# Kernel tuning notes

Hardware: AMD Instinct MI355X
Metric: run time of the kernel (lower is better)

Reference implementation:

```python
import jax, jax.numpy as jnp
import numpy as np

N, E = 50000, 800000          # nodes, edges
IN, H, C = 256, 4, 64          # in_channels, heads, per-head out channels
HID, OUT = 64, 40              # lin1 hidden, num classes
NEG_SLOPE = 0.2                # PyG GATConv default


def setup_inputs() -> dict:
    key = jax.random.key(0)
    ks = jax.random.split(key, 10)
    s = 0.05
    return {
        "x": jax.random.normal(ks[0], (N, IN), jnp.float32),
        "edge_index": jax.random.randint(ks[1], (2, E), 0, N, dtype=jnp.int64),
        "W": jax.random.normal(ks[2], (IN, H * C), jnp.float32) * s,     # GATConv lin (no bias)
        "att_src": jax.random.normal(ks[3], (H, C), jnp.float32) * s,
        "att_dst": jax.random.normal(ks[4], (H, C), jnp.float32) * s,
        "bias_conv": jnp.zeros((H * C,), jnp.float32),
        "W1": jax.random.normal(ks[5], (H * C, HID), jnp.float32) * s,
        "b1": jnp.zeros((HID,), jnp.float32),
        "W2": jax.random.normal(ks[6], (HID, OUT), jnp.float32) * s,
        "b2": jnp.zeros((OUT,), jnp.float32),
    }


def reference(x, edge_index, W, att_src, att_dst, bias_conv, W1, b1, W2, b2):
    n = x.shape[0]
    # PyG GATConv default: add self-loops (also guarantees no empty segments)
    loop = jnp.arange(n, dtype=edge_index.dtype)
    src = jnp.concatenate([edge_index[0], loop])  # [E+N]
    dst = jnp.concatenate([edge_index[1], loop])

    h = (x @ W).reshape(n, H, C)                         # [N,H,C]
    a_src = jnp.einsum('nhc,hc->nh', h, att_src)         # [N,H]
    a_dst = jnp.einsum('nhc,hc->nh', h, att_dst)

    # per-edge attention logits + segment softmax over incoming edges of dst
    e = jax.nn.leaky_relu(a_src[src] + a_dst[dst], NEG_SLOPE)   # [E+N,H]
    m = jax.ops.segment_max(e, dst, num_segments=n)             # [N,H]
    ex = jnp.exp(e - m[dst])
    denom = jax.ops.segment_sum(ex, dst, num_segments=n)
    alpha = ex / denom[dst]                                     # [E+N,H]

    # weighted scatter-aggregate of source features
    msg = alpha[:, :, None] * h[src]                            # [E+N,H,C]
    out = jax.ops.segment_sum(msg, dst, num_segments=n)         # [N,H,C]
    out = out.reshape(n, H * C) + bias_conv

    out = jax.nn.relu(out)              # .relu() after conv1 (dropout off in eval)
    out = jax.nn.relu(out @ W1 + b1)    # lin1 + relu
    return out @ W2 + b2                # lin2
```

## Files before the change

kernel.cpp:

```cpp
#include <hip/hip_runtime.h>
#include <math.h>

#define HEADS 4
#define CH 64
#define HC 256
#define SLOPE 0.2f

typedef __attribute__((ext_vector_type(8))) short bf16x8;
typedef __attribute__((ext_vector_type(4))) float f32x4;

__device__ __forceinline__ float4 ld4(const float* p){ return *(const float4*)p; }
__device__ __forceinline__ void st4(float* p, float4 v){ *(float4*)p = v; }
__device__ __forceinline__ float lrelu(float x){ return x > 0.f ? x : SLOPE * x; }
__device__ __forceinline__ unsigned short f2bf(float f){
  union { float f; unsigned int u; } v; v.f = f;
  unsigned int r = v.u + 0x7fffu + ((v.u >> 16) & 1u);
  return (unsigned short)(r >> 16);
}
__device__ __forceinline__ float bflo(unsigned int u){
  union { unsigned int u; float f; } v; v.u = u << 16; return v.f;
}
__device__ __forceinline__ float bfhi(unsigned int u){
  union { unsigned int u; float f; } v; v.u = u & 0xffff0000u; return v.f;
}
__device__ __forceinline__ void split2(float v, unsigned short& h, unsigned short& l){
  unsigned int u = __float_as_uint(v);
  h = (unsigned short)(u >> 16);
  float hf = __uint_as_float(u & 0xffff0000u);
  l = (unsigned short)(__float_as_uint(v - hf) >> 16);
}
__device__ __forceinline__ void dma16(const unsigned short* g, unsigned short* l){
  __builtin_amdgcn_global_load_lds(
      (const __attribute__((address_space(1))) unsigned int*)g,
      (__attribute__((address_space(3))) unsigned int*)l, 16, 0, 0);
}

__global__ __launch_bounds__(256) void k_pre(const float* __restrict__ x,
    const float* __restrict__ W, const float* __restrict__ W1, const float* __restrict__ W2,
    unsigned short* __restrict__ Ahi, unsigned short* __restrict__ Alo,
    unsigned short* __restrict__ Bhi, unsigned short* __restrict__ Blo,
    unsigned short* __restrict__ W1h, unsigned short* __restrict__ W1l,
    unsigned short* __restrict__ W2h, unsigned short* __restrict__ W2l,
    const int* __restrict__ ei, int* __restrict__ count,
    int nf4, int E, int nSplit) {
  int b = blockIdx.x, t = threadIdx.x;
  if (b < nSplit) {
    int idx = b*256 + t;
    if (idx < nf4) {
      float4 v = ld4(&x[(size_t)idx*4]);
      ushort4 h, l;
      split2(v.x, h.x, l.x); split2(v.y, h.y, l.y);
      split2(v.z, h.z, l.z); split2(v.w, h.w, l.w);
      *(ushort4*)&Ahi[(size_t)idx*4] = h;
      *(ushort4*)&Alo[(size_t)idx*4] = l;
    }
  } else if (b < nSplit + 256) {
    int nn = b - nSplit;
    unsigned short h, l;
    split2(W[(size_t)t*256 + nn], h, l);
    Bhi[(size_t)nn*256 + t] = h; Blo[(size_t)nn*256 + t] = l;
  } else if (b < nSplit + 320) {
    int nn = b - nSplit - 256;
    unsigned short h, l;
    split2(W1[(size_t)t*64 + nn], h, l);
    W1h[(size_t)nn*256 + t] = h; W1l[(size_t)nn*256 + t] = l;
  } else if (b < nSplit + 368) {
    if (t < 64) {
      int nn = b - nSplit - 320;
      float v = (nn < 40) ? W2[(size_t)t*40 + nn] : 0.f;
      unsigned short h, l;
      split2(v, h, l);
      W2h[(size_t)nn*64 + t] = h; W2l[(size_t)nn*64 + t] = l;
    }
  } else {
    int e = (b - nSplit - 368)*256 + t;
    if (e < E) atomicAdd(&count[ei[E+e]], 1);
  }
}

__global__ __launch_bounds__(256) void k_scan1(const int* __restrict__ count,
    int* __restrict__ excl, int* __restrict__ partial, int n) {
  __shared__ int sd[256];
  int blk = blockIdx.x, t = threadIdx.x;
  int i = blk*256 + t;
  int v = (i < n) ? count[i] + 1 : 0;
  sd[t] = v; __syncthreads();
  for (int off=1; off<256; off<<=1) {
    int xx = (t >= off) ? sd[t-off] : 0;
    __syncthreads();
    sd[t] += xx;
    __syncthreads();
  }
  if (i < n) excl[i] = sd[t] - v;
  if (t == 255) partial[blk] = sd[255];
}

__global__ __launch_bounds__(256) void k_scan23(int* __restrict__ row_start,
    int* __restrict__ cursor, const int* __restrict__ partial,
    const int* __restrict__ count, int n, int nb) {
  __shared__ int sd[256];
  int b = blockIdx.x, t = threadIdx.x;
  int v = (t < nb) ? partial[t] : 0;
  sd[t] = v; __syncthreads();
  for (int off=1; off<256; off<<=1) {
    int xx = (t >= off) ? sd[t-off] : 0;
    __syncthreads();
    sd[t] += xx;
    __syncthreads();
  }
  int pb = (b > 0) ? sd[b-1] : 0;
  int i = b*256 + t;
  if (i < n) {
    int vv = row_start[i] + pb;
    row_start[i] = vv;
    cursor[i] = vv;
    if (i == n-1) row_start[n] = vv + count[i] + 1;
  }
}

__global__ __launch_bounds__(256, 4) void k_gemmfill(const unsigned short* __restrict__ Ahi,
    const unsigned short* __restrict__ Alo,
    const unsigned short* __restrict__ Bhi_t, const unsigned short* __restrict__ Blo_t,
    unsigned short* __restrict__ hbf,
    const float* __restrict__ att_src, const float* __restrict__ att_dst,
    float* __restrict__ a_srcO, float* __restrict__ a_dstO, int M, int nGemm,
    const int* __restrict__ ei, int* __restrict__ cursor, int* __restrict__ csr,
    int E, int EN) {
  __shared__ __align__(16) unsigned short L[4*4096];
  int t = threadIdx.x;
  int b = blockIdx.x;
  if (b >= nGemm) {
    int base = (b - nGemm)*1024 + t;
    int e0 = base, e1 = base + 256, e2 = base + 512, e3 = base + 768;
    bool q0 = e0 < EN, q1 = e1 < EN, q2 = e2 < EN, q3 = e3 < EN;
    int s0=0,d0=0,s1=0,d1=0,s2=0,d2=0,s3=0,d3=0;
    if (q0) { if (e0 < E) { s0 = ei[e0]; d0 = ei[E+e0]; } else { s0 = e0-E; d0 = s0; } }
    if (q1) { if (e1 < E) { s1 = ei[e1]; d1 = ei[E+e1]; } else { s1 = e1-E; d1 = s1; } }
    if (q2) { if (e2 < E) { s2 = ei[e2]; d2 = ei[E+e2]; } else { s2 = e2-E; d2 = s2; } }
    if (q3) { if (e3 < E) { s3 = ei[e3]; d3 = ei[E+e3]; } else { s3 = e3-E; d3 = s3; } }
    if (q0) { int p = atomicAdd(&cursor[d0], 1); csr[p] = s0; }
    if (q1) { int p = atomicAdd(&cursor[d1], 1); csr[p] = s1; }
    if (q2) { int p = atomicAdd(&cursor[d2], 1); csr[p] = s2; }
    if (q3) { int p = atomicAdd(&cursor[d3], 1); csr[p] = s3; }
    return;
  }
  int lane = t & 63, w = t >> 6;
  int wr = w >> 1, wc = w & 1;
  int ln15 = lane & 15, lq = lane >> 4;
  int row0 = (b >> 1) * 128, col0 = (b & 1) * 128;

  f32x4 acc[4][4];
  #pragma unroll
  for (int i=0;i<4;i++)
    #pragma unroll
    for (int j=0;j<4;j++) acc[i][j] = (f32x4){0.f,0.f,0.f,0.f};

  int sA = w*128 + lane;
  int sB = sA + 64;
  int RA = sA>>3, uA = (sA&7)^(RA&7), idxA = (RA<<1)|(uA&1), segA = uA>>1;
  int RB = sB>>3, uB = (sB&7)^(RB&7), idxB = (RB<<1)|(uB&1), segB = uB>>1;
  size_t gA_a = (size_t)(row0+idxA)*256 + segA*8;
  size_t gA_b = (size_t)(row0+idxB)*256 + segB*8;
  size_t gB_a = (size_t)(col0+idxA)*256 + segA*8;
  size_t gB_b = (size_t)(col0+idxB)*256 + segB*8;
  int l0 = (w*128)*8, l1 = (w*128+64)*8;

  for (int c = 0; c < 8; c++) {
    int k0 = c*32;
    dma16(Ahi   + gA_a + k0, &L[0*4096 + l0]);
    dma16(Ahi   + gA_b + k0, &L[0*4096 + l1]);
    dma16(Alo   + gA_a + k0, &L[1*4096 + l0]);
    dma16(Alo   + gA_b + k0, &L[1*4096 + l1]);
    dma16(Bhi_t + gB_a + k0, &L[2*4096 + l0]);
    dma16(Bhi_t + gB_b + k0, &L[2*4096 + l1]);
    dma16(Blo_t + gB_a + k0, &L[3*4096 + l0]);
    dma16(Blo_t + gB_b + k0, &L[3*4096 + l1]);
    __syncthreads();

    bf16x8 bh[4], bl[4];
    #pragma unroll
    for (int j = 0; j < 4; j++) {
      int nn = wc*64 + j*16 + ln15;
      int R = nn >> 1, u = (lq << 1) | (nn & 1);
      int s = R*8 + (u ^ (R & 7));
      bh[j] = *(bf16x8*)&L[2*4096 + s*8];
      bl[j] = *(bf16x8*)&L[3*4096 + s*8];
    }
    #pragma unroll
    for (int i = 0; i < 4; i++) {
      int r = wr*64 + i*16 + ln15;
      int R = r >> 1, u = (lq << 1) | (r & 1);
      int s = R*8 + (u ^ (R & 7));
      bf16x8 ah = *(bf16x8*)&L[0*4096 + s*8];
      bf16x8 al = *(bf16x8*)&L[1*4096 + s*8];
      #pragma unroll
      for (int j = 0; j < 4; j++) {
        acc[i][j] = __builtin_amdgcn_mfma_f32_16x16x32_bf16(ah, bh[j], acc[i][j], 0,0,0);
        acc[i][j] = __builtin_amdgcn_mfma_f32_16x16x32_bf16(al, bh[j], acc[i][j], 0,0,0);
        acc[i][j] = __builtin_amdgcn_mfma_f32_16x16x32_bf16(ah, bl[j], acc[i][j], 0,0,0);
      }
    }
    __syncthreads();
  }
  unsigned short* hb2 = hbf + (size_t)(b & 1) * M * 128;
  #pragma unroll
  for (int i = 0; i < 4; i++) {
    #pragma unroll
    for (int r = 0; r < 4; r++) {
      int row = row0 + wr*64 + i*16 + lq*4 + r;
      if (row < M) {
        #pragma unroll
        for (int j = 0; j < 4; j++) {
          int col = wc*64 + j*16 + ln15;
          hb2[(size_t)row*128 + col] = f2bf(acc[i][j][r]);
        }
      }
    }
  }
  int head = (b & 1)*2 + wc;
  float asv[4], adv[4];
  #pragma unroll
  for (int j=0;j<4;j++){
    asv[j] = att_src[head*CH + j*16 + ln15];
    adv[j] = att_dst[head*CH + j*16 + ln15];
  }
  #pragma unroll
  for (int i = 0; i < 4; i++) {
    #pragma unroll
    for (int r = 0; r < 4; r++) {
      float ps = acc[i][0][r]*asv[0] + acc[i][1][r]*asv[1]
               + acc[i][2][r]*asv[2] + acc[i][3][r]*asv[3];
      float pd = acc[i][0][r]*adv[0] + acc[i][1][r]*adv[1]
               + acc[i][2][r]*adv[2] + acc[i][3][r]*adv[3];
      #pragma unroll
      for (int m=8; m>=1; m>>=1) { ps += __shfl_xor(ps, m); pd += __shfl_xor(pd, m); }
      if (ln15 == 0) {
        int row = row0 + wr*64 + i*16 + lq*4 + r;
        if (row < M) { a_srcO[row*4+head] = ps; a_dstO[row*4+head] = pd; }
      }
    }
  }
}

__global__ __launch_bounds__(256) void k_gat(const unsigned short* __restrict__ hbf,
    const float* __restrict__ a_src, const float* __restrict__ a_dst,
    const int* __restrict__ row_start, const int* __restrict__ csr,
    const float* __restrict__ bias, unsigned short* __restrict__ outbf,
    int N, int nBlk) {
  int w = threadIdx.x >> 6, lane = threadIdx.x & 63;
  int q = lane >> 4, cl = lane & 15;
  int pass = (blockIdx.x >= nBlk) ? 1 : 0;
  int blk = blockIdx.x - pass*nBlk;
  int n = blk*16 + w*4 + q;
  int c0 = cl * 8;
  int hd = cl >> 3;
  int eb = q * 16;
  const unsigned short* hb = hbf + (size_t)pass * N * 128;

  __shared__ float s_p[4][64][2];

  float2 ad = *(const float2*)&a_dst[(size_t)n*4 + pass*2];
  float dsum = 0.f;
  float acc[8];
  #pragma unroll
  for (int k=0;k<8;k++) acc[k]=0.f;

  int beg = row_start[n];
  int deg = row_start[n+1] - beg;
  int dm = max(deg, __shfl_xor(deg, 16));
  dm = max(dm, __shfl_xor(dm, 32));

  for (int cb = 0; cb < dm; cb += 16) {
    int cnt = min(16, deg - cb);
    int cm  = min(16, dm - cb);
    int s = 0;
    float p0 = 0.f, p1 = 0.f;
    if (cl < cnt) {
      s = csr[beg + cb + cl];
      float2 as = *(const float2*)&a_src[(size_t)s*4 + pass*2];
      p0 = __expf(lrelu(as.x + ad.x));
      p1 = __expf(lrelu(as.y + ad.y));
    }
    *(float2*)&s_p[w][eb + cl][0] = make_float2(p0, p1);

    bool v0 = 0 < cnt, v1 = 1 < cnt, v2 = 2 < cnt, v3 = 3 < cnt;
    uint4 u0 = make_uint4(0,0,0,0), u1 = u0, u2 = u0, u3 = u0;
    int ss;
    ss = __shfl(s, eb + 0); if (v0) u0 = *(const uint4*)&hb[(size_t)ss*128 + c0];
    ss = __shfl(s, eb + 1); if (v1) u1 = *(const uint4*)&hb[(size_t)ss*128 + c0];
    ss = __shfl(s, eb + 2); if (v2) u2 = *(const uint4*)&hb[(size_t)ss*128 + c0];
    ss = __shfl(s, eb + 3); if (v3) u3 = *(const uint4*)&hb[(size_t)ss*128 + c0];
    for (int g = 0; g < cm; g += 4) {
      int f0 = g+4, f1 = g+5, f2 = g+6, f3 = g+7;
      bool w0 = f0 < cnt, w1 = f1 < cnt, w2 = f2 < cnt, w3 = f3 < cnt;
      uint4 t0 = make_uint4(0,0,0,0), t1 = t0, t2 = t0, t3 = t0;
      ss = __shfl(s, eb + (f0 & 15)); if (w0) t0 = *(const uint4*)&hb[(size_t)ss*128 + c0];
      ss = __shfl(s, eb + (f1 & 15)); if (w1) t1 = *(const uint4*)&hb[(size_t)ss*128 + c0];
      ss = __shfl(s, eb + (f2 & 15)); if (w2) t2 = *(const uint4*)&hb[(size_t)ss*128 + c0];
      ss = __shfl(s, eb + (f3 & 15)); if (w3) t3 = *(const uint4*)&hb[(size_t)ss*128 + c0];
      if (v0) {
        float pw = s_p[w][eb + g    ][hd]; dsum += pw;
        acc[0] += pw*bflo(u0.x); acc[1] += pw*bfhi(u0.x);
        acc[2] += pw*bflo(u0.y); acc[3] += pw*bfhi(u0.y);
        acc[4] += pw*bflo(u0.z); acc[5] += pw*bfhi(u0.z);
        acc[6] += pw*bflo(u0.w); acc[7] += pw*bfhi(u0.w);
      }
      if (v1) {
        float pw = s_p[w][eb + g + 1][hd]; dsum += pw;
        acc[0] += pw*bflo(u1.x); acc[1] += pw*bfhi(u1.x);
        acc[2] += pw*bflo(u1.y); acc[3] += pw*bfhi(u1.y);
        acc[4] += pw*bflo(u1.z); acc[5] += pw*bfhi(u1.z);
        acc[6] += pw*bflo(u1.w); acc[7] += pw*bfhi(u1.w);
      }
      if (v2) {
        float pw = s_p[w][eb + g + 2][hd]; dsum += pw;
        acc[0] += pw*bflo(u2.x); acc[1] += pw*bfhi(u2.x);
        acc[2] += pw*bflo(u2.y); acc[3] += pw*bfhi(u2.y);
        acc[4] += pw*bflo(u2.z); acc[5] += pw*bfhi(u2.z);
        acc[6] += pw*bflo(u2.w); acc[7] += pw*bfhi(u2.w);
      }
      if (v3) {
        float pw = s_p[w][eb + g + 3][hd]; dsum += pw;
        acc[0] += pw*bflo(u3.x); acc[1] += pw*bfhi(u3.x);
        acc[2] += pw*bflo(u3.y); acc[3] += pw*bfhi(u3.y);
        acc[4] += pw*bflo(u3.z); acc[5] += pw*bfhi(u3.z);
        acc[6] += pw*bflo(u3.w); acc[7] += pw*bfhi(u3.w);
      }
      u0 = t0; u1 = t1; u2 = t2; u3 = t3;
      v0 = w0; v1 = w1; v2 = w2; v3 = w3;
    }
  }
  float inv = 1.f / dsum;
  float4 b0 = ld4(&bias[pass*128 + c0]);
  float4 b1 = ld4(&bias[pass*128 + c0 + 4]);
  uint4 o;
  o.x = (unsigned)f2bf(fmaxf(acc[0]*inv + b0.x, 0.f))
      | ((unsigned)f2bf(fmaxf(acc[1]*inv + b0.y, 0.f)) << 16);
  o.y = (unsigned)f2bf(fmaxf(acc[2]*inv + b0.z, 0.f))
      | ((unsigned)f2bf(fmaxf(acc[3]*inv + b0.w, 0.f)) << 16);
  o.z = (unsigned)f2bf(fmaxf(acc[4]*inv + b1.x, 0.f))
      | ((unsigned)f2bf(fmaxf(acc[5]*inv + b1.y, 0.f)) << 16);
  o.w = (unsigned)f2bf(fmaxf(acc[6]*inv + b1.z, 0.f))
      | ((unsigned)f2bf(fmaxf(acc[7]*inv + b1.w, 0.f)) << 16);
  *(uint4*)&outbf[(size_t)n*HC + pass*128 + c0] = o;
}

__global__ __launch_bounds__(256) void k_mlp(const unsigned short* __restrict__ Cbf,
    const unsigned short* __restrict__ W1h, const unsigned short* __restrict__ W1l,
    const unsigned short* __restrict__ W2h, const unsigned short* __restrict__ W2l,
    const float* __restrict__ b1, const float* __restrict__ b2,
    float* __restrict__ out, int M) {
  __shared__ __align__(16) unsigned short Abuf[4096];
  __shared__ __align__(16) unsigned short Hs[128*72];
  int t = threadIdx.x, lane = t & 63, w = t >> 6;
  int ln15 = lane & 15, lq = lane >> 4;
  int row0 = blockIdx.x * 128;

  f32x4 acc1[2][4];
  #pragma unroll
  for (int i=0;i<2;i++)
    #pragma unroll
    for (int j=0;j<4;j++) acc1[i][j] = (f32x4){0.f,0.f,0.f,0.f};

  int sA = w*64 + lane;
  int sB = 256 + w*64 + lane;
  int rA = sA >> 2, segA = (sA & 3) ^ ((rA >> 1) & 3);
  int rB = sB >> 2, segB = (sB & 3) ^ ((rB >> 1) & 3);
  size_t gA = (size_t)(row0 + rA) * 256 + segA*8;
  size_t gB = (size_t)(row0 + rB) * 256 + segB*8;
  int lA = (w*64)*8, lB = (256 + w*64)*8;

  for (int c = 0; c < 8; c++) {
    int k0 = c*32;
    dma16(Cbf + gA + k0, &Abuf[lA]);
    dma16(Cbf + gB + k0, &Abuf[lB]);
    __syncthreads();
    bf16x8 a[2];
    #pragma unroll
    for (int i = 0; i < 2; i++) {
      int r = w*32 + i*16 + ln15;
      int s = r*4 + (lq ^ ((r >> 1) & 3));
      a[i] = *(bf16x8*)&Abuf[s*8];
    }
    #pragma unroll
    for (int j = 0; j < 4; j++) {
      int n = j*16 + ln15;
      int k = k0 + lq*8;
      bf16x8 bh = *(const bf16x8*)&W1h[(size_t)n*256 + k];
      bf16x8 bl = *(const bf16x8*)&W1l[(size_t)n*256 + k];
      #pragma unroll
      for (int i = 0; i < 2; i++) {
        acc1[i][j] = __builtin_amdgcn_mfma_f32_16x16x32_bf16(a[i], bh, acc1[i][j], 0,0,0);
        acc1[i][j] = __builtin_amdgcn_mfma_f32_16x16x32_bf16(a[i], bl, acc1[i][j], 0,0,0);
      }
    }
    __syncthreads();
  }
  #pragma unroll
  for (int j = 0; j < 4; j++) {
    int col = j*16 + ln15;
    float bv = b1[col];
    #pragma unroll
    for (int i = 0; i < 2; i++) {
      #pragma unroll
      for (int r = 0; r < 4; r++) {
        int row = w*32 + i*16 + lq*4 + r;
        Hs[row*72 + col] = f2bf(fmaxf(acc1[i][j][r] + bv, 0.f));
      }
    }
  }
  f32x4 acc2[2][3];
  #pragma unroll
  for (int i=0;i<2;i++)
    #pragma unroll
    for (int j=0;j<3;j++) acc2[i][j] = (f32x4){0.f,0.f,0.f,0.f};
  #pragma unroll
  for (int kf = 0; kf < 2; kf++) {
    bf16x8 a2[2];
    #pragma unroll
    for (int i = 0; i < 2; i++) {
      int m = w*32 + i*16 + ln15;
      a2[i] = *(bf16x8*)&Hs[m*72 + kf*32 + lq*8];
    }
    #pragma unroll
    for (int j = 0; j < 3; j++) {
      int n = j*16 + ln15;
      int k = kf*32 + lq*8;
      bf16x8 wh = *(const bf16x8*)&W2h[(size_t)n*64 + k];
      bf16x8 wl = *(const bf16x8*)&W2l[(size_t)n*64 + k];
      #pragma unroll
      for (int i = 0; i < 2; i++) {
        acc2[i][j] = __builtin_amdgcn_mfma_f32_16x16x32_bf16(a2[i], wh, acc2[i][j], 0,0,0);
        acc2[i][j] = __builtin_amdgcn_mfma_f32_16x16x32_bf16(a2[i], wl, acc2[i][j], 0,0,0);
      }
    }
  }
  #pragma unroll
  for (int j = 0; j < 3; j++) {
    int col = j*16 + ln15;
    if (col < 40) {
      float bv = b2[col];
      #pragma unroll
      for (int i = 0; i < 2; i++) {
        #pragma unroll
        for (int r = 0; r < 4; r++) {
          int row = row0 + w*32 + i*16 + lq*4 + r;
          if (row < M) out[(size_t)row*40 + col] = acc2[i][j][r] + bv;
        }
      }
    }
  }
}

extern "C" void kernel_launch(void* const* d_in, const int* in_sizes, int n_in,
                              void* d_out, int out_size, void* d_ws, size_t ws_size,
                              hipStream_t stream) {
  const int Nn = in_sizes[0] / HC;
  const int E  = in_sizes[1] / 2;
  const int Mpad = (Nn + 127) & ~127;
  const float* x        = (const float*)d_in[0];
  const int*   ei       = (const int*)d_in[1];
  const float* W        = (const float*)d_in[2];
  const float* att_src  = (const float*)d_in[3];
  const float* att_dst  = (const float*)d_in[4];
  const float* biasconv = (const float*)d_in[5];
  const float* W1       = (const float*)d_in[6];
  const float* b1       = (const float*)d_in[7];
  const float* W2       = (const float*)d_in[8];
  const float* b2       = (const float*)d_in[9];
  float* out = (float*)d_out;

  size_t off = 0;
  auto alloc = [&](size_t bytes)->void* {
    void* p = (void*)((char*)d_ws + off);
    off += (bytes + 255) & ~(size_t)255;
    return p;
  };
  unsigned short* hbf = (unsigned short*)alloc((size_t)Nn*HC*sizeof(unsigned short));
  void* ublk = alloc((size_t)Mpad*HC*sizeof(float));
  unsigned short* Ahi = (unsigned short*)ublk;
  unsigned short* Alo = Ahi + (size_t)Mpad*HC;
  unsigned short* outc = (unsigned short*)ublk;
  unsigned short* Bhi = (unsigned short*)alloc((size_t)256*256*sizeof(unsigned short));
  unsigned short* Blo = (unsigned short*)alloc((size_t)256*256*sizeof(unsigned short));
  unsigned short* W1h = (unsigned short*)alloc((size_t)64*256*sizeof(unsigned short));
  unsigned short* W1l = (unsigned short*)alloc((size_t)64*256*sizeof(unsigned short));
  unsigned short* W2h = (unsigned short*)alloc((size_t)48*64*sizeof(unsigned short));
  unsigned short* W2l = (unsigned short*)alloc((size_t)48*64*sizeof(unsigned short));
  float* a_src_v  = (float*)alloc((size_t)Nn*4*sizeof(float));
  float* a_dst_v  = (float*)alloc((size_t)Nn*4*sizeof(float));
  int*   count    = (int*)alloc((size_t)Nn*sizeof(int));
  int*   rowstart = (int*)alloc((size_t)(Nn+1)*sizeof(int));
  int*   cursor   = (int*)alloc((size_t)Nn*sizeof(int));
  int*   partial  = (int*)alloc(256*sizeof(int));
  int*   csr      = (int*)alloc((size_t)(E+Nn)*sizeof(int));
  (void)ws_size; (void)n_in; (void)out_size;

  dim3 blk(256);
  int nf4 = Nn*64;
  int nSplit = (nf4 + 255)/256;
  int nCnt = (E + 255)/256;
  int nb = (Nn + 255)/256;
  int nGemm = 2 * (Mpad/128);
  int EN = E + Nn;
  int nFill = (EN + 1023)/1024;
  int nBlkGat = Nn/16;

  hipMemsetAsync(count, 0, (size_t)Nn*sizeof(int), stream);
  k_pre<<<dim3(nSplit + 368 + nCnt), blk, 0, stream>>>(x, W, W1, W2,
      Ahi, Alo, Bhi, Blo, W1h, W1l, W2h, W2l, ei, count, nf4, E, nSplit);
  k_scan1<<<dim3(nb), blk, 0, stream>>>(count, rowstart, partial, Nn);
  k_scan23<<<dim3(nb), blk, 0, stream>>>(rowstart, cursor, partial, count, Nn, nb);
  k_gemmfill<<<dim3(nGemm + nFill), blk, 0, stream>>>(Ahi, Alo, Bhi, Blo, hbf,
      att_src, att_dst, a_src_v, a_dst_v, Nn, nGemm, ei, cursor, csr, E, EN);
  k_gat<<<dim3(2*nBlkGat), blk, 0, stream>>>(hbf, a_src_v, a_dst_v,
                                             rowstart, csr, biasconv, outc, Nn, nBlkGat);
  k_mlp<<<dim3(Mpad/128), blk, 0, stream>>>(outc, W1h, W1l, W2h, W2l, b1, b2, out, Nn);
}
```

Baseline: 304.1 us.

## Fuse x hi/lo bf16 split into GEMM A-tile load, reorder fill blocks

The separate pre-pass that split x into hi/lo bf16 arrays in global memory is removed. The GEMM now loads fp32 x directly, splits it in registers and writes the swizzled LDS tile itself, which avoids a full write and re-read of the split copies. The CSR fill blocks are placed first in the grid and each handles 2048 edges instead of 1024. In exchange the A operand no longer goes through the async global-to-LDS DMA, so the GEMM's load path now includes synchronous loads plus conversion ALU work.

```diff
diff --git a/kernel.cpp b/kernel.cpp
--- a/kernel.cpp
+++ b/kernel.cpp
@@ -7,6 +7,7 @@
 #define SLOPE 0.2f
 
 typedef __attribute__((ext_vector_type(8))) short bf16x8;
+typedef __attribute__((ext_vector_type(8))) unsigned short u16x8;
 typedef __attribute__((ext_vector_type(4))) float f32x4;
 
 __device__ __forceinline__ float4 ld4(const float* p){ return *(const float4*)p; }
@@ -35,45 +36,33 @@
       (__attribute__((address_space(3))) unsigned int*)l, 16, 0, 0);
 }
 
-__global__ __launch_bounds__(256) void k_pre(const float* __restrict__ x,
+__global__ __launch_bounds__(256) void k_pre(
     const float* __restrict__ W, const float* __restrict__ W1, const float* __restrict__ W2,
-    unsigned short* __restrict__ Ahi, unsigned short* __restrict__ Alo,
     unsigned short* __restrict__ Bhi, unsigned short* __restrict__ Blo,
     unsigned short* __restrict__ W1h, unsigned short* __restrict__ W1l,
     unsigned short* __restrict__ W2h, unsigned short* __restrict__ W2l,
-    const int* __restrict__ ei, int* __restrict__ count,
-    int nf4, int E, int nSplit) {
+    const int* __restrict__ ei, int* __restrict__ count, int E) {
   int b = blockIdx.x, t = threadIdx.x;
-  if (b < nSplit) {
-    int idx = b*256 + t;
-    if (idx < nf4) {
-      float4 v = ld4(&x[(size_t)idx*4]);
-      ushort4 h, l;
-      split2(v.x, h.x, l.x); split2(v.y, h.y, l.y);
-      split2(v.z, h.z, l.z); split2(v.w, h.w, l.w);
-      *(ushort4*)&Ahi[(size_t)idx*4] = h;
-      *(ushort4*)&Alo[(size_t)idx*4] = l;
-    }
-  } else if (b < nSplit + 256) {
-    int nn = b - nSplit;
+  if (b < 256) {
+    int nn = b;
     unsigned short h, l;
     split2(W[(size_t)t*256 + nn], h, l);
     Bhi[(size_t)nn*256 + t] = h; Blo[(size_t)nn*256 + t] = l;
-  } else if (b < nSplit + 320) {
-    int nn = b - nSplit - 256;
+  } else if (b < 320) {
+    int nn = b - 256;
     unsigned short h, l;
     split2(W1[(size_t)t*64 + nn], h, l);
     W1h[(size_t)nn*256 + t] = h; W1l[(size_t)nn*256 + t] = l;
-  } else if (b < nSplit + 368) {
+  } else if (b < 368) {
     if (t < 64) {
-      int nn = b - nSplit - 320;
+      int nn = b - 320;
       float v = (nn < 40) ? W2[(size_t)t*40 + nn] : 0.f;
       unsigned short h, l;
       split2(v, h, l);
       W2h[(size_t)nn*64 + t] = h; W2l[(size_t)nn*64 + t] = l;
     }
   } else {
-    int e = (b - nSplit - 368)*256 + t;
+    int e = (b - 368)*256 + t;
     if (e < E) atomicAdd(&count[ei[E+e]], 1);
   }
 }
@@ -118,36 +107,46 @@
   }
 }
 
-__global__ __launch_bounds__(256, 4) void k_gemmfill(const unsigned short* __restrict__ Ahi,
-    const unsigned short* __restrict__ Alo,
+__global__ __launch_bounds__(256, 4) void k_gemmfill(const float* __restrict__ x,
     const unsigned short* __restrict__ Bhi_t, const unsigned short* __restrict__ Blo_t,
     unsigned short* __restrict__ hbf,
     const float* __restrict__ att_src, const float* __restrict__ att_dst,
-    float* __restrict__ a_srcO, float* __restrict__ a_dstO, int M, int nGemm,
+    float* __restrict__ a_srcO, float* __restrict__ a_dstO, int M, int nFill,
     const int* __restrict__ ei, int* __restrict__ cursor, int* __restrict__ csr,
     int E, int EN) {
   __shared__ __align__(16) unsigned short L[4*4096];
   int t = threadIdx.x;
   int b = blockIdx.x;
-  if (b >= nGemm) {
-    int base = (b - nGemm)*1024 + t;
-    int e0 = base, e1 = base + 256, e2 = base + 512, e3 = base + 768;
-    bool q0 = e0 < EN, q1 = e1 < EN, q2 = e2 < EN, q3 = e3 < EN;
+  if (b < nFill) {
+    int base = b*2048 + t;
     int s0=0,d0=0,s1=0,d1=0,s2=0,d2=0,s3=0,d3=0;
-    if (q0) { if (e0 < E) { s0 = ei[e0]; d0 = ei[E+e0]; } else { s0 = e0-E; d0 = s0; } }
-    if (q1) { if (e1 < E) { s1 = ei[e1]; d1 = ei[E+e1]; } else { s1 = e1-E; d1 = s1; } }
-    if (q2) { if (e2 < E) { s2 = ei[e2]; d2 = ei[E+e2]; } else { s2 = e2-E; d2 = s2; } }
-    if (q3) { if (e3 < E) { s3 = ei[e3]; d3 = ei[E+e3]; } else { s3 = e3-E; d3 = s3; } }
+    int s4=0,d4=0,s5=0,d5=0,s6=0,d6=0,s7=0,d7=0;
+    int e0=base, e1=base+256, e2=base+512, e3=base+768;
+    int e4=base+1024, e5=base+1280, e6=base+1536, e7=base+1792;
+    bool q0=e0<EN,q1=e1<EN,q2=e2<EN,q3=e3<EN,q4=e4<EN,q5=e5<EN,q6=e6<EN,q7=e7<EN;
+    if (q0) { if (e0<E) { s0=ei[e0]; d0=ei[E+e0]; } else { s0=e0-E; d0=s0; } }
+    if (q1) { if (e1<E) { s1=ei[e1]; d1=ei[E+e1]; } else { s1=e1-E; d1=s1; } }
+    if (q2) { if (e2<E) { s2=ei[e2]; d2=ei[E+e2]; } else { s2=e2-E; d2=s2; } }
+    if (q3) { if (e3<E) { s3=ei[e3]; d3=ei[E+e3]; } else { s3=e3-E; d3=s3; } }
+    if (q4) { if (e4<E) { s4=ei[e4]; d4=ei[E+e4]; } else { s4=e4-E; d4=s4; } }
+    if (q5) { if (e5<E) { s5=ei[e5]; d5=ei[E+e5]; } else { s5=e5-E; d5=s5; } }
+    if (q6) { if (e6<E) { s6=ei[e6]; d6=ei[E+e6]; } else { s6=e6-E; d6=s6; } }
+    if (q7) { if (e7<E) { s7=ei[e7]; d7=ei[E+e7]; } else { s7=e7-E; d7=s7; } }
     if (q0) { int p = atomicAdd(&cursor[d0], 1); csr[p] = s0; }
     if (q1) { int p = atomicAdd(&cursor[d1], 1); csr[p] = s1; }
     if (q2) { int p = atomicAdd(&cursor[d2], 1); csr[p] = s2; }
     if (q3) { int p = atomicAdd(&cursor[d3], 1); csr[p] = s3; }
+    if (q4) { int p = atomicAdd(&cursor[d4], 1); csr[p] = s4; }
+    if (q5) { int p = atomicAdd(&cursor[d5], 1); csr[p] = s5; }
+    if (q6) { int p = atomicAdd(&cursor[d6], 1); csr[p] = s6; }
+    if (q7) { int p = atomicAdd(&cursor[d7], 1); csr[p] = s7; }
     return;
   }
+  int gb = b - nFill;
   int lane = t & 63, w = t >> 6;
   int wr = w >> 1, wc = w & 1;
   int ln15 = lane & 15, lq = lane >> 4;
-  int row0 = (b >> 1) * 128, col0 = (b & 1) * 128;
+  int row0 = (gb >> 1) * 128, col0 = (gb & 1) * 128;
 
   f32x4 acc[4][4];
   #pragma unroll
@@ -159,22 +158,53 @@
   int sB = sA + 64;
   int RA = sA>>3, uA = (sA&7)^(RA&7), idxA = (RA<<1)|(uA&1), segA = uA>>1;
   int RB = sB>>3, uB = (sB&7)^(RB&7), idxB = (RB<<1)|(uB&1), segB = uB>>1;
-  size_t gA_a = (size_t)(row0+idxA)*256 + segA*8;
-  size_t gA_b = (size_t)(row0+idxB)*256 + segB*8;
   size_t gB_a = (size_t)(col0+idxA)*256 + segA*8;
   size_t gB_b = (size_t)(col0+idxB)*256 + segB*8;
   int l0 = (w*128)*8, l1 = (w*128+64)*8;
 
+  int ar = t >> 1, akh = t & 1;
+  int arow = row0 + ar;
+  bool avalid = arow < M;
+  const float* xp = &x[(size_t)arow*256 + akh*16];
+  int aR = ar >> 1;
+  int u0w = ((2*akh+0) << 1) | (ar & 1);
+  int u1w = ((2*akh+1) << 1) | (ar & 1);
+  int as0 = aR*8 + (u0w ^ (aR & 7));
+  int as1 = aR*8 + (u1w ^ (aR & 7));
+
   for (int c = 0; c < 8; c++) {
     int k0 = c*32;
-    dma16(Ahi   + gA_a + k0, &L[0*4096 + l0]);
-    dma16(Ahi   + gA_b + k0, &L[0*4096 + l1]);
-    dma16(Alo   + gA_a + k0, &L[1*4096 + l0]);
-    dma16(Alo   + gA_b + k0, &L[1*4096 + l1]);
     dma16(Bhi_t + gB_a + k0, &L[2*4096 + l0]);
     dma16(Bhi_t + gB_b + k0, &L[2*4096 + l1]);
     dma16(Blo_t + gB_a + k0, &L[3*4096 + l0]);
     dma16(Blo_t + gB_b + k0, &L[3*4096 + l1]);
+    float4 f0 = make_float4(0,0,0,0), f1 = f0, f2 = f0, f3 = f0;
+    if (avalid) {
+      const float* xc = xp + k0;
+      f0 = ld4(xc); f1 = ld4(xc+4); f2 = ld4(xc+8); f3 = ld4(xc+12);
+    }
+    u16x8 h0, l0v, h1, l1v;
+    unsigned short hh, ll;
+    split2(f0.x,hh,ll); h0[0]=hh; l0v[0]=ll;
+    split2(f0.y,hh,ll); h0[1]=hh; l0v[1]=ll;
+    split2(f0.z,hh,ll); h0[2]=hh; l0v[2]=ll;
+    split2(f0.w,hh,ll); h0[3]=hh; l0v[3]=ll;
+    split2(f1.x,hh,ll); h0[4]=hh; l0v[4]=ll;
+    split2(f1.y,hh,ll); h0[5]=hh; l0v[5]=ll;
+    split2(f1.z,hh,ll); h0[6]=hh; l0v[6]=ll;
+    split2(f1.w,hh,ll); h0[7]=hh; l0v[7]=ll;
+    split2(f2.x,hh,ll); h1[0]=hh; l1v[0]=ll;
+    split2(f2.y,hh,ll); h1[1]=hh; l1v[1]=ll;
+    split2(f2.z,hh,ll); h1[2]=hh; l1v[2]=ll;
+    split2(f2.w,hh,ll); h1[3]=hh; l1v[3]=ll;
+    split2(f3.x,hh,ll); h1[4]=hh; l1v[4]=ll;
+    split2(f3.y,hh,ll); h1[5]=hh; l1v[5]=ll;
+    split2(f3.z,hh,ll); h1[6]=hh; l1v[6]=ll;
+    split2(f3.w,hh,ll); h1[7]=hh; l1v[7]=ll;
+    *(u16x8*)&L[0*4096 + as0*8] = h0;
+    *(u16x8*)&L[1*4096 + as0*8] = l0v;
+    *(u16x8*)&L[0*4096 + as1*8] = h1;
+    *(u16x8*)&L[1*4096 + as1*8] = l1v;
     __syncthreads();
 
     bf16x8 bh[4], bl[4];
@@ -202,7 +232,7 @@
     }
     __syncthreads();
   }
-  unsigned short* hb2 = hbf + (size_t)(b & 1) * M * 128;
+  unsigned short* hb2 = hbf + (size_t)(gb & 1) * M * 128;
   #pragma unroll
   for (int i = 0; i < 4; i++) {
     #pragma unroll
@@ -217,7 +247,7 @@
       }
     }
   }
-  int head = (b & 1)*2 + wc;
+  int head = (gb & 1)*2 + wc;
   float asv[4], adv[4];
   #pragma unroll
   for (int j=0;j<4;j++){
@@ -476,11 +506,8 @@
     off += (bytes + 255) & ~(size_t)255;
     return p;
   };
-  unsigned short* hbf = (unsigned short*)alloc((size_t)Nn*HC*sizeof(unsigned short));
-  void* ublk = alloc((size_t)Mpad*HC*sizeof(float));
-  unsigned short* Ahi = (unsigned short*)ublk;
-  unsigned short* Alo = Ahi + (size_t)Mpad*HC;
-  unsigned short* outc = (unsigned short*)ublk;
+  unsigned short* hbf  = (unsigned short*)alloc((size_t)Nn*HC*sizeof(unsigned short));
+  unsigned short* outc = (unsigned short*)alloc((size_t)Mpad*HC*sizeof(unsigned short));
   unsigned short* Bhi = (unsigned short*)alloc((size_t)256*256*sizeof(unsigned short));
   unsigned short* Blo = (unsigned short*)alloc((size_t)256*256*sizeof(unsigned short));
   unsigned short* W1h = (unsigned short*)alloc((size_t)64*256*sizeof(unsigned short));
@@ -497,22 +524,20 @@
   (void)ws_size; (void)n_in; (void)out_size;
 
   dim3 blk(256);
-  int nf4 = Nn*64;
-  int nSplit = (nf4 + 255)/256;
   int nCnt = (E + 255)/256;
   int nb = (Nn + 255)/256;
   int nGemm = 2 * (Mpad/128);
   int EN = E + Nn;
-  int nFill = (EN + 1023)/1024;
+  int nFill = (EN + 2047)/2048;
   int nBlkGat = Nn/16;
 
   hipMemsetAsync(count, 0, (size_t)Nn*sizeof(int), stream);
-  k_pre<<<dim3(nSplit + 368 + nCnt), blk, 0, stream>>>(x, W, W1, W2,
-      Ahi, Alo, Bhi, Blo, W1h, W1l, W2h, W2l, ei, count, nf4, E, nSplit);
+  k_pre<<<dim3(368 + nCnt), blk, 0, stream>>>(W, W1, W2,
+      Bhi, Blo, W1h, W1l, W2h, W2l, ei, count, E);
   k_scan1<<<dim3(nb), blk, 0, stream>>>(count, rowstart, partial, Nn);
   k_scan23<<<dim3(nb), blk, 0, stream>>>(rowstart, cursor, partial, count, Nn, nb);
-  k_gemmfill<<<dim3(nGemm + nFill), blk, 0, stream>>>(Ahi, Alo, Bhi, Blo, hbf,
-      att_src, att_dst, a_src_v, a_dst_v, Nn, nGemm, ei, cursor, csr, E, EN);
+  k_gemmfill<<<dim3(nFill + nGemm), blk, 0, stream>>>(x, Bhi, Blo, hbf,
+      att_src, att_dst, a_src_v, a_dst_v, Nn, nFill, ei, cursor, csr, E, EN);
   k_gat<<<dim3(2*nBlkGat), blk, 0, stream>>>(hbf, a_src_v, a_dst_v,
                                              rowstart, csr, biasconv, outc, Nn, nBlkGat);
   k_mlp<<<dim3(Mpad/128), blk, 0, stream>>>(outc, W1h, W1l, W2h, W2l, b1, b2, out, Nn);
```

After: 292.6 us. 1.04x faster.
